# Optimization experiments

Measured on AMD Instinct MI355X. Metric: run time of the kernel, lower is better.

The kernel has to match this reference:

```python
import jax, jax.numpy as jnp
import numpy as np

B, S, N, M = 2, 4, 4096, 4096


def setup_inputs() -> dict:
    key = jax.random.key(0)
    k1, k2 = jax.random.split(key)
    output_points = jax.random.normal(k1, (B, S, N, 3), dtype=jnp.float32)
    target_points = jax.random.normal(k2, (B, S, M, 3), dtype=jnp.float32)
    return {"output_points": output_points, "target_points": target_points, "n_samples": N}


def _chamfer(x, y):
    # x: [B,S,N,3], y: [B,S,M,3]; squared-Euclidean bidirectional NN distances
    x2 = jnp.sum(x * x, axis=-1)                      # [B,S,N]
    y2 = jnp.sum(y * y, axis=-1)                      # [B,S,M]
    xy = jnp.einsum('bsnd,bsmd->bsnm', x, y)          # [B,S,N,M]
    d = x2[..., :, None] + y2[..., None, :] - 2.0 * xy
    dist1 = jnp.min(d, axis=-1)                       # [B,S,N] out->tgt NN
    dist2 = jnp.min(d, axis=-2)                       # [B,S,M] tgt->out NN
    return dist1, dist2


def reference(output_points, target_points, n_samples):
    # n_samples already applied (clouds are pre-sampled to fixed size)
    dist1, dist2 = _chamfer(output_points, target_points)
    # per-(b,s) combined distance: mean(dist1) + mean(dist2)
    combined = jnp.mean(dist1, axis=-1) + jnp.mean(dist2, axis=-1)  # [B,S]
    chamfer_distances_tensor = combined.T                            # [S,B]
    chamfer_distances = jnp.mean(chamfer_distances_tensor, axis=1)   # [S] (dict s -> mean over batch)
    return chamfer_distances, chamfer_distances_tensor
```

## Files before the change

### kernel.cpp

```cpp
#include <hip/hip_runtime.h>

constexpr int Sn = 4;
constexpr int Nn = 4096;
constexpr int Mn = 4096;
constexpr int NS2 = 16;
constexpr int APT = 8;
constexpr int NBC = 32;
constexpr int BCHUNK = Mn / NBC;


__global__ __launch_bounds__(256) void chamfer_partial(
    const float* __restrict__ X,
    const float* __restrict__ Y,
    unsigned int* __restrict__ rowmin)
{
    constexpr int ATILE = APT * 256;

    __shared__ float4 ldsB[BCHUNK];

    const int at    = blockIdx.x;
    const int bc    = blockIdx.y;
    const int z     = blockIdx.z;
    const int slice = z & 7;
    const int dir   = z >> 3;
    const int tid   = threadIdx.x;

    const float* A  = (dir == 0 ? X : Y) + (size_t)slice * (Nn * 3);
    const float* Bp = (dir == 0 ? Y : X) + (size_t)slice * (Mn * 3) + bc * (BCHUNK * 3);

    float ax[APT], ay[APT], az[APT], acc[APT];
    #pragma unroll
    for (int j = 0; j < APT; ++j) {
        const int n = at * ATILE + j * 256 + tid;
        ax[j] = A[n * 3 + 0];
        ay[j] = A[n * 3 + 1];
        az[j] = A[n * 3 + 2];
        acc[j] = 3.4e38f;
    }

    for (int p = tid; p < BCHUNK; p += 256) {
        float bx = Bp[p * 3 + 0], by = Bp[p * 3 + 1], bz = Bp[p * 3 + 2];
        ldsB[p] = make_float4(-2.0f * bx, -2.0f * by, -2.0f * bz,
                              bx * bx + by * by + bz * bz);
    }
    __syncthreads();

    #pragma unroll 4
    for (int m = 0; m < BCHUNK; m += 2) {
        const float4 b0 = ldsB[m + 0];
        const float4 b1 = ldsB[m + 1];
        #pragma unroll
        for (int j = 0; j < APT; ++j) {
            float d0 = fmaf(ax[j], b0.x, fmaf(ay[j], b0.y, fmaf(az[j], b0.z, b0.w)));
            float d1 = fmaf(ax[j], b1.x, fmaf(ay[j], b1.y, fmaf(az[j], b1.z, b1.w)));
            acc[j] = fminf(fminf(acc[j], d0), d1);
        }
    }

    unsigned int* dst = rowmin + (size_t)z * Nn + at * ATILE;
    #pragma unroll
    for (int j = 0; j < APT; ++j) {
        const float a2 = ax[j] * ax[j] + ay[j] * ay[j] + az[j] * az[j];
        const float d  = fmaxf(acc[j] + a2, 0.0f);
        atomicMin(&dst[j * 256 + tid], __float_as_uint(d));
    }
}

__global__ __launch_bounds__(256) void chamfer_rowsum(
    const unsigned int* __restrict__ rowmin, float* __restrict__ sums)
{
    const int z   = blockIdx.x;
    const int tid = threadIdx.x;
    const unsigned int* p = rowmin + (size_t)z * Nn;

    float s = 0.0f;
    #pragma unroll
    for (int i = tid; i < Nn; i += 256) s += __uint_as_float(p[i]);

    s += __shfl_down(s, 32);
    s += __shfl_down(s, 16);
    s += __shfl_down(s, 8);
    s += __shfl_down(s, 4);
    s += __shfl_down(s, 2);
    s += __shfl_down(s, 1);

    __shared__ float red[4];
    if ((tid & 63) == 0) red[tid >> 6] = s;
    __syncthreads();
    if (tid == 0) sums[z] = red[0] + red[1] + red[2] + red[3];
}

__global__ __launch_bounds__(64) void chamfer_finalize(
    const float* __restrict__ sums, float* __restrict__ out)
{
    const int tid = threadIdx.x;
    if (tid < 8) {
        const int s = tid >> 1, b = tid & 1;
        const int l = b * Sn + s;
        out[4 + s * 2 + b] = sums[l] * (1.0f / Nn) + sums[8 + l] * (1.0f / Mn);
    } else if (tid < 12) {
        const int s = tid - 8;
        float c0 = sums[0 * Sn + s] * (1.0f / Nn) + sums[8 + 0 * Sn + s] * (1.0f / Mn);
        float c1 = sums[1 * Sn + s] * (1.0f / Nn) + sums[8 + 1 * Sn + s] * (1.0f / Mn);
        out[s] = 0.5f * (c0 + c1);
    }
}

extern "C" void kernel_launch(void* const* d_in, const int* in_sizes, int n_in,
                              void* d_out, int out_size, void* d_ws, size_t ws_size,
                              hipStream_t stream) {
    const float* X = (const float*)d_in[0];
    const float* Y = (const float*)d_in[1];
    float* out = (float*)d_out;

    unsigned int* rowmin = (unsigned int*)d_ws;
    float* sums = (float*)(rowmin + (size_t)NS2 * Nn);

    hipMemsetAsync(rowmin, 0x7F, (size_t)NS2 * Nn * sizeof(unsigned int), stream);

    dim3 grid(Nn / (APT * 256), NBC, NS2);
    chamfer_partial<<<grid, 256, 0, stream>>>(X, Y, rowmin);
    chamfer_rowsum<<<NS2, 256, 0, stream>>>(rowmin, sums);
    chamfer_finalize<<<1, 64, 0, stream>>>(sums, out);
}
```

Measured before the change: 36.76 us.

## Compute pairwise distances with split-bf16 MFMA instead of scalar FMA

Adds a pack kernel that splits each coordinate and squared norm into high and low bf16 parts, arranged so that a single 16x16x32 bf16 MFMA yields the full squared distance at roughly fp32 accuracy. The main kernel keeps row minima from the MFMA outputs, reduces them with cross-lane shuffles, and writes two per-half partial minima instead of using atomicMin. This removes the memset and atomics and moves the arithmetic from vector ALUs onto matrix cores. The cost is an extra pack pass and workspace traffic, half of each wave's lanes sit idle feeding zero inputs, and the split-bf16 approximation may lose some precision.

```diff
diff --git a/kernel.cpp b/kernel.cpp
--- a/kernel.cpp
+++ b/kernel.cpp
@@ -2,106 +2,177 @@
 
 constexpr int Sn = 4;
 constexpr int Nn = 4096;
-constexpr int Mn = 4096;
 constexpr int NS2 = 16;
-constexpr int APT = 8;
-constexpr int NBC = 32;
-constexpr int BCHUNK = Mn / NBC;
 
+typedef __attribute__((ext_vector_type(8))) short short8v;
+typedef __attribute__((ext_vector_type(4))) float f32x4;
 
-__global__ __launch_bounds__(256) void chamfer_partial(
-    const float* __restrict__ X,
-    const float* __restrict__ Y,
-    unsigned int* __restrict__ rowmin)
+constexpr size_t PACK_F4 = (size_t)2 * 8 * 4096 * 2;
+
+__device__ inline unsigned short f2bf(float x) {
+    unsigned int u = __float_as_uint(x);
+    unsigned int r = u + 0x7FFFu + ((u >> 16) & 1u);
+    return (unsigned short)(r >> 16);
+}
+__device__ inline float bf2f(unsigned short h) {
+    return __uint_as_float(((unsigned int)h) << 16);
+}
+__device__ inline float4 pack8(unsigned short s0, unsigned short s1, unsigned short s2,
+                               unsigned short s3, unsigned short s4, unsigned short s5,
+                               unsigned short s6, unsigned short s7) {
+    union { unsigned short s[8]; float4 v; } u;
+    u.s[0]=s0; u.s[1]=s1; u.s[2]=s2; u.s[3]=s3;
+    u.s[4]=s4; u.s[5]=s5; u.s[6]=s6; u.s[7]=s7;
+    return u.v;
+}
+
+__global__ __launch_bounds__(256) void chamfer_pack(
+    const float* __restrict__ X, const float* __restrict__ Y,
+    float4* __restrict__ Apack, float4* __restrict__ Bpack)
 {
-    constexpr int ATILE = APT * 256;
+    const int idx  = blockIdx.x * 256 + threadIdx.x;
+    const int side = idx >> 15;
+    const int rem  = idx & 32767;
+    const float* src = (side == 0 ? X : Y) + (size_t)rem * 3;
+    const float x = src[0], y = src[1], z = src[2];
 
-    __shared__ float4 ldsB[BCHUNK];
+    const unsigned short hx = f2bf(x), hy = f2bf(y), hz = f2bf(z);
+    const float fx = bf2f(hx), fy = bf2f(hy), fz = bf2f(hz);
+    const unsigned short lx = f2bf(x - fx), ly = f2bf(y - fy), lz = f2bf(z - fz);
+    const float n2 = x * x + y * y + z * z;
+    const unsigned short n2h = f2bf(n2);
+    const unsigned short n2l = f2bf(n2 - bf2f(n2h));
+    const unsigned short one = 0x3F80;
+    const unsigned short mhx = f2bf(-2.0f * bf2f(hx)), mhy = f2bf(-2.0f * bf2f(hy)),
+                         mhz = f2bf(-2.0f * bf2f(hz));
+    const unsigned short mlx = f2bf(-2.0f * bf2f(lx)), mly = f2bf(-2.0f * bf2f(ly)),
+                         mlz = f2bf(-2.0f * bf2f(lz));
 
-    const int at    = blockIdx.x;
-    const int bc    = blockIdx.y;
-    const int z     = blockIdx.z;
-    const int slice = z & 7;
-    const int dir   = z >> 3;
-    const int tid   = threadIdx.x;
+    const size_t base = (size_t)idx * 2;
+    Apack[base + 0] = pack8(hx, hy, hz, lx, ly, lz, n2h, n2l);
+    Apack[base + 1] = pack8(hx, hy, hz, lx, ly, lz, one, one);
+    Bpack[base + 0] = pack8(mhx, mhy, mhz, mhx, mhy, mhz, one, one);
+    Bpack[base + 1] = pack8(mlx, mly, mlz, mlx, mly, mlz, n2h, n2l);
+}
 
-    const float* A  = (dir == 0 ? X : Y) + (size_t)slice * (Nn * 3);
-    const float* Bp = (dir == 0 ? Y : X) + (size_t)slice * (Mn * 3) + bc * (BCHUNK * 3);
+__global__ __launch_bounds__(256) void chamfer_mfma(
+    const float4* __restrict__ Apack, const float4* __restrict__ Bpack,
+    float* __restrict__ rowhalf)
+{
+    const int band = blockIdx.x;
+    const int half = blockIdx.y;
+    const int zz   = blockIdx.z;
+    const int p    = zz >> 3;
+    const int slice= zz & 7;
+    const int tid  = threadIdx.x;
+    const int w    = tid >> 6;
+    const int cc   = tid & 15;
+    const int cg   = (tid & 63) >> 4;
+    const bool act = (cg < 2);
 
-    float ax[APT], ay[APT], az[APT], acc[APT];
-    #pragma unroll
-    for (int j = 0; j < APT; ++j) {
-        const int n = at * ATILE + j * 256 + tid;
-        ax[j] = A[n * 3 + 0];
-        ay[j] = A[n * 3 + 1];
-        az[j] = A[n * 3 + 2];
-        acc[j] = 3.4e38f;
+    const float4* Ap = Apack + ((size_t)(p * 8 + slice) * 4096) * 2;
+    const float4* Bp = Bpack + ((size_t)((1 - p) * 8 + slice) * 4096) * 2;
+
+    short8v a0 = {0,0,0,0,0,0,0,0}, a1 = {0,0,0,0,0,0,0,0};
+    const int r0 = band * 128 + w * 32 + cc;
+    if (act) {
+        float4 t0 = Ap[(size_t)r0 * 2 + cg];
+        float4 t1 = Ap[(size_t)(r0 + 16) * 2 + cg];
+        a0 = *(short8v*)&t0;
+        a1 = *(short8v*)&t1;
     }
 
-    for (int p = tid; p < BCHUNK; p += 256) {
-        float bx = Bp[p * 3 + 0], by = Bp[p * 3 + 1], bz = Bp[p * 3 + 2];
-        ldsB[p] = make_float4(-2.0f * bx, -2.0f * by, -2.0f * bz,
-                              bx * bx + by * by + bz * bz);
-    }
-    __syncthreads();
+    __shared__ float4 lds[2][1024];
 
-    #pragma unroll 4
-    for (int m = 0; m < BCHUNK; m += 2) {
-        const float4 b0 = ldsB[m + 0];
-        const float4 b1 = ldsB[m + 1];
-        #pragma unroll
-        for (int j = 0; j < APT; ++j) {
-            float d0 = fmaf(ax[j], b0.x, fmaf(ay[j], b0.y, fmaf(az[j], b0.z, b0.w)));
-            float d1 = fmaf(ax[j], b1.x, fmaf(ay[j], b1.y, fmaf(az[j], b1.z, b1.w)));
-            acc[j] = fminf(fminf(acc[j], d0), d1);
+    f32x4 rmin0, rmin1;
+    rmin0[0]=rmin0[1]=rmin0[2]=rmin0[3]=3.4e38f;
+    rmin1[0]=rmin1[1]=rmin1[2]=rmin1[3]=3.4e38f;
+
+    for (int chunk = 0; chunk < 2; ++chunk) {
+        const int colbase = half * 2048 + chunk * 1024;
+        if (chunk) __syncthreads();
+        for (int i = tid; i < 2048; i += 256) {
+            const int col = i >> 1, g = i & 1;
+            lds[g][col] = Bp[(size_t)(colbase + col) * 2 + g];
+        }
+        __syncthreads();
+
+        #pragma unroll 4
+        for (int step = 0; step < 64; ++step) {
+            short8v bf = {0,0,0,0,0,0,0,0};
+            if (act) {
+                float4 t = lds[cg][step * 16 + cc];
+                bf = *(short8v*)&t;
+            }
+            const f32x4 zero = {0.0f, 0.0f, 0.0f, 0.0f};
+            f32x4 acc0 = __builtin_amdgcn_mfma_f32_16x16x32_bf16(a0, bf, zero, 0, 0, 0);
+            f32x4 acc1 = __builtin_amdgcn_mfma_f32_16x16x32_bf16(a1, bf, zero, 0, 0, 0);
+            rmin0[0]=fminf(rmin0[0],acc0[0]); rmin0[1]=fminf(rmin0[1],acc0[1]);
+            rmin0[2]=fminf(rmin0[2],acc0[2]); rmin0[3]=fminf(rmin0[3],acc0[3]);
+            rmin1[0]=fminf(rmin1[0],acc1[0]); rmin1[1]=fminf(rmin1[1],acc1[1]);
+            rmin1[2]=fminf(rmin1[2],acc1[2]); rmin1[3]=fminf(rmin1[3],acc1[3]);
         }
     }
 
-    unsigned int* dst = rowmin + (size_t)z * Nn + at * ATILE;
     #pragma unroll
-    for (int j = 0; j < APT; ++j) {
-        const float a2 = ax[j] * ax[j] + ay[j] * ay[j] + az[j] * az[j];
-        const float d  = fmaxf(acc[j] + a2, 0.0f);
-        atomicMin(&dst[j * 256 + tid], __float_as_uint(d));
+    for (int off = 1; off <= 8; off <<= 1) {
+        rmin0[0]=fminf(rmin0[0],__shfl_xor(rmin0[0],off)); rmin0[1]=fminf(rmin0[1],__shfl_xor(rmin0[1],off));
+        rmin0[2]=fminf(rmin0[2],__shfl_xor(rmin0[2],off)); rmin0[3]=fminf(rmin0[3],__shfl_xor(rmin0[3],off));
+        rmin1[0]=fminf(rmin1[0],__shfl_xor(rmin1[0],off)); rmin1[1]=fminf(rmin1[1],__shfl_xor(rmin1[1],off));
+        rmin1[2]=fminf(rmin1[2],__shfl_xor(rmin1[2],off)); rmin1[3]=fminf(rmin1[3],__shfl_xor(rmin1[3],off));
+    }
+    if (cc == 0) {
+        float* dst = rowhalf + ((size_t)half * NS2 + zz) * Nn + band * 128 + w * 32;
+        #pragma unroll
+        for (int r = 0; r < 4; ++r) {
+            dst[4 * cg + r]      = rmin0[r];
+            dst[16 + 4 * cg + r] = rmin1[r];
+        }
     }
 }
 
 __global__ __launch_bounds__(256) void chamfer_rowsum(
-    const unsigned int* __restrict__ rowmin, float* __restrict__ sums)
+    const float* __restrict__ rowhalf, float* __restrict__ sums2)
 {
     const int z   = blockIdx.x;
+    const int c   = blockIdx.y;
     const int tid = threadIdx.x;
-    const unsigned int* p = rowmin + (size_t)z * Nn;
+    const float* p0 = rowhalf + (size_t)z * Nn;
+    const float* p1 = rowhalf + (size_t)(NS2 + z) * Nn;
 
     float s = 0.0f;
-    #pragma unroll
-    for (int i = tid; i < Nn; i += 256) s += __uint_as_float(p[i]);
+    for (int i = c * 512 + tid; i < (c + 1) * 512; i += 256)
+        s += fminf(p0[i], p1[i]);
 
-    s += __shfl_down(s, 32);
-    s += __shfl_down(s, 16);
-    s += __shfl_down(s, 8);
-    s += __shfl_down(s, 4);
-    s += __shfl_down(s, 2);
-    s += __shfl_down(s, 1);
+    s += __shfl_down(s, 32); s += __shfl_down(s, 16); s += __shfl_down(s, 8);
+    s += __shfl_down(s, 4);  s += __shfl_down(s, 2);  s += __shfl_down(s, 1);
 
     __shared__ float red[4];
     if ((tid & 63) == 0) red[tid >> 6] = s;
     __syncthreads();
-    if (tid == 0) sums[z] = red[0] + red[1] + red[2] + red[3];
+    if (tid == 0) sums2[z * 8 + c] = red[0] + red[1] + red[2] + red[3];
 }
 
 __global__ __launch_bounds__(64) void chamfer_finalize(
-    const float* __restrict__ sums, float* __restrict__ out)
+    const float* __restrict__ sums2, float* __restrict__ out)
 {
     const int tid = threadIdx.x;
+    __shared__ float tot[NS2];
+    if (tid < NS2) {
+        float t = 0.0f;
+        #pragma unroll
+        for (int c = 0; c < 8; ++c) t += sums2[tid * 8 + c];
+        tot[tid] = t;
+    }
+    __syncthreads();
     if (tid < 8) {
         const int s = tid >> 1, b = tid & 1;
         const int l = b * Sn + s;
-        out[4 + s * 2 + b] = sums[l] * (1.0f / Nn) + sums[8 + l] * (1.0f / Mn);
+        out[4 + s * 2 + b] = tot[l] * (1.0f / Nn) + tot[8 + l] * (1.0f / Nn);
     } else if (tid < 12) {
         const int s = tid - 8;
-        float c0 = sums[0 * Sn + s] * (1.0f / Nn) + sums[8 + 0 * Sn + s] * (1.0f / Mn);
-        float c1 = sums[1 * Sn + s] * (1.0f / Nn) + sums[8 + 1 * Sn + s] * (1.0f / Mn);
+        float c0 = tot[0 * Sn + s] * (1.0f / Nn) + tot[8 + 0 * Sn + s] * (1.0f / Nn);
+        float c1 = tot[1 * Sn + s] * (1.0f / Nn) + tot[8 + 1 * Sn + s] * (1.0f / Nn);
         out[s] = 0.5f * (c0 + c1);
     }
 }
@@ -113,13 +184,13 @@
     const float* Y = (const float*)d_in[1];
     float* out = (float*)d_out;
 
-    unsigned int* rowmin = (unsigned int*)d_ws;
-    float* sums = (float*)(rowmin + (size_t)NS2 * Nn);
+    float4* Apack  = (float4*)d_ws;
+    float4* Bpack  = Apack + PACK_F4;
+    float* rowhalf = (float*)(Bpack + PACK_F4);
+    float* sums2   = rowhalf + (size_t)2 * NS2 * Nn;
 
-    hipMemsetAsync(rowmin, 0x7F, (size_t)NS2 * Nn * sizeof(unsigned int), stream);
-
-    dim3 grid(Nn / (APT * 256), NBC, NS2);
-    chamfer_partial<<<grid, 256, 0, stream>>>(X, Y, rowmin);
-    chamfer_rowsum<<<NS2, 256, 0, stream>>>(rowmin, sums);
-    chamfer_finalize<<<1, 64, 0, stream>>>(sums, out);
+    chamfer_pack<<<65536 / 256, 256, 0, stream>>>(X, Y, Apack, Bpack);
+    chamfer_mfma<<<dim3(32, 2, NS2), 256, 0, stream>>>(Apack, Bpack, rowhalf);
+    chamfer_rowsum<<<dim3(NS2, 8), 256, 0, stream>>>(rowhalf, sums2);
+    chamfer_finalize<<<1, 64, 0, stream>>>(sums2, out);
 }
```

New measurement: 36.25 us. Within noise of the previous version (-1.4%).
